# Kernel optimization log

Hardware: AMD Instinct MI355X
Metric: run time of the kernel (lower is better)

The kernel has to match this reference:

```python
import jax, jax.numpy as jnp
import numpy as np

NUM_GRAPHS = 64

def _sage(x, edge_index, Wl, bl, Wr):
    # PyG SAGEConv (mean aggr): out = lin_l(mean_{j in N(i)} x_j) + lin_r(x_i)
    src, dst = edge_index[0], edge_index[1]
    n = x.shape[0]
    summed = jax.ops.segment_sum(x[src], dst, num_segments=n)        # [N,F]
    deg = jax.ops.segment_sum(jnp.ones_like(src, dtype=x.dtype), dst, num_segments=n)
    agg = summed / jnp.maximum(deg, 1.0)[:, None]
    return agg @ Wl.T + bl + x @ Wr.T

def setup_inputs() -> dict:
    key = jax.random.key(0)
    ks = jax.random.split(key, 12)
    N, E, F, H = 50000, 600000, 128, 128
    x = jax.random.normal(ks[0], (N, F), dtype=jnp.float32)
    edge_index = jax.random.randint(ks[1], (2, E), 0, N, dtype=jnp.int64)
    batch = jnp.sort(jax.random.randint(ks[2], (N,), 0, NUM_GRAPHS, dtype=jnp.int64))
    s = lambda fan_in: 1.0 / np.sqrt(fan_in)
    return {
        "x": x, "edge_index": edge_index, "batch": batch,
        "W1l": jax.random.uniform(ks[3], (H, F), minval=-s(F), maxval=s(F)),
        "b1l": jnp.zeros((H,), jnp.float32),
        "W1r": jax.random.uniform(ks[4], (H, F), minval=-s(F), maxval=s(F)),
        "W2l": jax.random.uniform(ks[5], (H, H), minval=-s(H), maxval=s(H)),
        "b2l": jnp.zeros((H,), jnp.float32),
        "W2r": jax.random.uniform(ks[6], (H, H), minval=-s(H), maxval=s(H)),
        "Wc1": jax.random.uniform(ks[7], (H, H), minval=-s(H), maxval=s(H)),
        "bc1": jax.random.uniform(ks[8], (H,), minval=-s(H), maxval=s(H)),
        "Wc2": jax.random.uniform(ks[9], (1, H), minval=-s(H), maxval=s(H)),
        "bc2": jax.random.uniform(ks[10], (1,), minval=-s(H), maxval=s(H)),
    }

def reference(x, edge_index, batch, W1l, b1l, W1r, W2l, b2l, W2r, Wc1, bc1, Wc2, bc2):
    h = jax.nn.relu(_sage(x, edge_index, W1l, b1l, W1r))
    h = jax.nn.relu(_sage(h, edge_index, W2l, b2l, W2r))
    # global mean pool per graph
    gsum = jax.ops.segment_sum(h, batch, num_segments=NUM_GRAPHS)
    gcnt = jax.ops.segment_sum(jnp.ones((h.shape[0],), h.dtype), batch, num_segments=NUM_GRAPHS)
    gemb = gsum / jnp.maximum(gcnt, 1.0)[:, None]                    # [G,H]
    # classifier MLP (dropout = identity in eval)
    z = jax.nn.relu(gemb @ Wc1.T + bc1)
    out = (z @ Wc2.T + bc2).squeeze(-1)                              # [G]
    return out
```

## Files before the change

### kernel.cpp

```cpp
#include <hip/hip_runtime.h>


typedef __attribute__((ext_vector_type(8))) short bf16x8;
typedef __attribute__((ext_vector_type(8))) unsigned short ushort8;
typedef __attribute__((ext_vector_type(4))) float f32x4;

#define HBLK 4096

__device__ inline unsigned short f2bf(float f) {
  unsigned u = __float_as_uint(f);
  u += 0x7fff + ((u >> 16) & 1);
  return (unsigned short)(u >> 16);
}
__device__ inline float bf2f(unsigned short h) { return __uint_as_float(((unsigned)h) << 16); }


__device__ inline void wprep_body(int id, const float* __restrict__ Wl, const float* __restrict__ Wr,
                                  unsigned short* __restrict__ Bpre) {
  if (id >= 4096) return;
  int kk = id >> 9;
  int ct = (id >> 6) & 7;
  int l  = id & 63;
  int colIdx = ct * 16 + (l & 15);
  int k0 = kk * 32 + (l >> 4) * 8;
  const float* W = (k0 < 128) ? Wl : Wr;
  int kb = k0 & 127;
#pragma unroll
  for (int j = 0; j < 8; ++j) {
    float v = W[colIdx * 128 + kb + j];
    unsigned short h = f2bf(v);
    size_t bh = (size_t)kk * 8192 + ((size_t)ct * 64 + l) * 8 + j;
    Bpre[bh] = h;
    Bpre[bh + 4096] = f2bf(v - bf2f(h));
  }
}

__global__ __launch_bounds__(256) void k_prep(
    const float* __restrict__ x, unsigned short* __restrict__ xbf, int total,
    const float* __restrict__ W1l, const float* __restrict__ W1r, unsigned short* __restrict__ Bpre1,
    const float* __restrict__ W2l, const float* __restrict__ W2r, unsigned short* __restrict__ Bpre2,
    const int* __restrict__ batch, int* __restrict__ gcnt, float* __restrict__ gsum, int N,
    const int* __restrict__ ei, int* __restrict__ bhist, int E,
    int nTobf, int nEblk) {
  __shared__ int h[256];
  int b = blockIdx.x;
  int tid = threadIdx.x;
  if (b < nTobf) {
    int i = (b * 256 + tid) * 4;
    if (i + 3 < total) {
      float4 v = *(const float4*)(x + i);
      ushort4 p;
      p.x = f2bf(v.x); p.y = f2bf(v.y); p.z = f2bf(v.z); p.w = f2bf(v.w);
      *(ushort4*)(xbf + i) = p;
    } else {
      for (int k = 0; k < 4 && i + k < total; ++k) xbf[i + k] = f2bf(x[i + k]);
    }
  } else if (b < nTobf + 16) {
    wprep_body((b - nTobf) * 256 + tid, W1l, W1r, Bpre1);
  } else if (b < nTobf + 32) {
    wprep_body((b - nTobf - 16) * 256 + tid, W2l, W2r, Bpre2);
  } else if (b < nTobf + 32 + nEblk) {
    int eb = b - nTobf - 32;
    h[tid] = 0;
    __syncthreads();
    int base = eb * HBLK;
    int end = min(base + HBLK, E);
    for (int e = base + tid; e < end; e += 256) atomicAdd(&h[ei[E + e] >> 8], 1);
    __syncthreads();
    bhist[eb * 256 + tid] = h[tid];
  } else {
    for (int i = tid; i < 64 * 128; i += 256) gsum[i] = 0.f;
    if (tid < 64) {
      int g = tid;
      int lo = 0, hi = N;
      while (lo < hi) { int mid = (lo + hi) >> 1; if (batch[mid] < g) lo = mid + 1; else hi = mid; }
      int a = lo;
      lo = 0; hi = N;
      while (lo < hi) { int mid = (lo + hi) >> 1; if (batch[mid] < g + 1) lo = mid + 1; else hi = mid; }
      gcnt[g] = lo - a;
    }
  }
}


__global__ __launch_bounds__(256) void k_bscan(int* __restrict__ bhist, int* __restrict__ bukbase,
                                               int nblk) {
  __shared__ int s[256];
  int buk = blockIdx.x;
  int t = threadIdx.x;
  int sum = 0;
  for (int b = 0; b < nblk; ++b) sum += bhist[b * 256 + t];
  s[t] = sum;
  __syncthreads();
  for (int d = 1; d < 256; d <<= 1) {
    int v = (t >= d) ? s[t - d] : 0;
    __syncthreads();
    s[t] += v;
    __syncthreads();
  }
  int myBase = (buk == 0) ? 0 : s[buk - 1];
  int tot = s[255];
  __syncthreads();
  int c = (t < nblk) ? bhist[t * 256 + buk] : 0;
  s[t] = c;
  __syncthreads();
  for (int d = 1; d < 256; d <<= 1) {
    int v = (t >= d) ? s[t - d] : 0;
    __syncthreads();
    s[t] += v;
    __syncthreads();
  }
  if (t < nblk) bhist[t * 256 + buk] = myBase + s[t] - c;
  if (t == 0) bukbase[buk] = myBase;
  if (buk == 255 && t == 1) bukbase[256] = tot;
}

__global__ __launch_bounds__(256) void k_scat(const int* __restrict__ ei, const int* __restrict__ bhist,
                                              unsigned* __restrict__ ebuk, int E) {
  __shared__ int cur[256];
  int tid = threadIdx.x;
  cur[tid] = bhist[blockIdx.x * 256 + tid];
  __syncthreads();
  int base = blockIdx.x * HBLK;
  int end = min(base + HBLK, E);
  for (int e = base + tid; e < end; e += 256) {
    int d = ei[E + e];
    int srcv = ei[e];
    int p = atomicAdd(&cur[d >> 8], 1);
    ebuk[p] = ((unsigned)(d & 255) << 24) | (unsigned)srcv;
  }
}

__global__ __launch_bounds__(256) void k_bucket(const unsigned* __restrict__ ebuk,
                                                const int* __restrict__ bukbase,
                                                int* __restrict__ off, int* __restrict__ colv,
                                                int N, int E) {
  __shared__ int h[256];
  __shared__ int cur[256];
  __shared__ int sc[256];
  int tid = threadIdx.x;
  int buk = blockIdx.x;
  int b0 = bukbase[buk], b1 = bukbase[buk + 1];
  h[tid] = 0;
  __syncthreads();
  for (int i = b0 + tid; i < b1; i += 256) atomicAdd(&h[ebuk[i] >> 24], 1);
  __syncthreads();
  int my = h[tid];
  sc[tid] = my;
  __syncthreads();
  for (int d = 1; d < 256; d <<= 1) {
    int v = (tid >= d) ? sc[tid - d] : 0;
    __syncthreads();
    sc[tid] += v;
    __syncthreads();
  }
  int excl = sc[tid] - my;
  cur[tid] = excl;
  int node = buk * 256 + tid;
  if (node < N) off[node] = b0 + excl;
  if (buk == gridDim.x - 1 && tid == 0) off[N] = E;
  __syncthreads();
  for (int i = b0 + tid; i < b1; i += 256) {
    unsigned v = ebuk[i];
    int p = atomicAdd(&cur[v >> 24], 1);
    colv[b0 + p] = (int)(v & 0xFFFFFFu);
  }
}


__global__ __launch_bounds__(256) void k_agg_bf(const unsigned short* __restrict__ Xbf,
                                                const int* __restrict__ off, const int* __restrict__ col,
                                                unsigned short* __restrict__ Tbf, int N) {
  int wid = (blockIdx.x * 256 + threadIdx.x) >> 6;
  int ln = threadIdx.x & 63;
  if (wid >= N) return;
  int o0 = off[wid], o1 = off[wid + 1];
  int deg = o1 - o0;
  int rs = ln >> 4, fs = ln & 15;
  float acc[8];
#pragma unroll
  for (int j = 0; j < 8; ++j) acc[j] = 0.f;

  for (int base = 0; base < deg; base += 16) {
#pragma unroll
    for (int u = 0; u < 4; ++u) {
      int n = base + u * 4 + rs;
      if (n < deg) {
        int idx = col[o0 + n];
        ushort8 q = *(const ushort8*)(Xbf + (size_t)idx * 128 + fs * 8);
#pragma unroll
        for (int j = 0; j < 8; ++j) acc[j] += bf2f(q[j]);
      }
    }
  }
#pragma unroll
  for (int j = 0; j < 8; ++j) {
    acc[j] += __shfl_xor(acc[j], 16);
    acc[j] += __shfl_xor(acc[j], 32);
  }
  if (rs == 0) {
    float sc = 1.0f / (float)max(deg, 1);
    unsigned short w[8];
#pragma unroll
    for (int j = 0; j < 8; ++j) w[j] = f2bf(acc[j] * sc);
    uint4 uw;
    uw.x = (unsigned)w[0] | ((unsigned)w[1] << 16);
    uw.y = (unsigned)w[2] | ((unsigned)w[3] << 16);
    uw.z = (unsigned)w[4] | ((unsigned)w[5] << 16);
    uw.w = (unsigned)w[6] | ((unsigned)w[7] << 16);
    *(uint4*)(Tbf + (size_t)wid * 128 + fs * 8) = uw;
  }
}


__global__ __launch_bounds__(256) void k_lin2(
    const unsigned short* __restrict__ Agg,
    const unsigned short* __restrict__ Self,
    const unsigned short* __restrict__ Bpre,
    const float* __restrict__ bias,
    unsigned short* __restrict__ OUTbf,
    const int* __restrict__ batch, float* __restrict__ gsum,
    int N, int mode) {
  __shared__ float ps[128];
  int tid = threadIdx.x;
  int wv = tid >> 6, ln = tid & 63;
  int rowBase = blockIdx.x * 64;
  int kq = (ln >> 4) * 8;
  int rsel = ln & 15;
  int c0 = wv * 2;

  f32x4 acc[4][2];
#pragma unroll
  for (int rg = 0; rg < 4; ++rg) {
    acc[rg][0] = (f32x4){0.f, 0.f, 0.f, 0.f};
    acc[rg][1] = (f32x4){0.f, 0.f, 0.f, 0.f};
  }

#pragma unroll
  for (int kk = 0; kk < 8; ++kk) {
    const unsigned short* S = (kk < 4) ? Agg : Self;
    int kOff = (kk & 3) * 32 + kq;
    const unsigned short* Bk = Bpre + (size_t)kk * 8192;
    bf16x8 bh0 = *(const bf16x8*)(Bk + ((size_t)c0 * 64 + ln) * 8);
    bf16x8 bl0 = *(const bf16x8*)(Bk + 4096 + ((size_t)c0 * 64 + ln) * 8);
    bf16x8 bh1 = *(const bf16x8*)(Bk + ((size_t)(c0 + 1) * 64 + ln) * 8);
    bf16x8 bl1 = *(const bf16x8*)(Bk + 4096 + ((size_t)(c0 + 1) * 64 + ln) * 8);
    bf16x8 ah[4];
#pragma unroll
    for (int rg = 0; rg < 4; ++rg) {
      int row = min(rowBase + rg * 16 + rsel, N - 1);
      ah[rg] = *(const bf16x8*)(S + (size_t)row * 128 + kOff);
    }
#pragma unroll
    for (int rg = 0; rg < 4; ++rg) {
      acc[rg][0] = __builtin_amdgcn_mfma_f32_16x16x32_bf16(ah[rg], bh0, acc[rg][0], 0, 0, 0);
      acc[rg][0] = __builtin_amdgcn_mfma_f32_16x16x32_bf16(ah[rg], bl0, acc[rg][0], 0, 0, 0);
      acc[rg][1] = __builtin_amdgcn_mfma_f32_16x16x32_bf16(ah[rg], bh1, acc[rg][1], 0, 0, 0);
      acc[rg][1] = __builtin_amdgcn_mfma_f32_16x16x32_bf16(ah[rg], bl1, acc[rg][1], 0, 0, 0);
    }
  }

  int lcol = ln & 15;
  int rsub = (ln >> 4) * 4;
#pragma unroll
  for (int c = 0; c < 2; ++c) {
    float b = bias[(wv * 2 + c) * 16 + lcol];
#pragma unroll
    for (int rg = 0; rg < 4; ++rg)
#pragma unroll
      for (int r = 0; r < 4; ++r) acc[rg][c][r] = fmaxf(acc[rg][c][r] + b, 0.f);
  }

  if (mode == 0) {
#pragma unroll
    for (int rg = 0; rg < 4; ++rg)
#pragma unroll
      for (int r = 0; r < 4; ++r) {
        int row = rowBase + rg * 16 + rsub + r;
        if (row < N) {
          OUTbf[(size_t)row * 128 + (wv * 2 + 0) * 16 + lcol] = f2bf(acc[rg][0][r]);
          OUTbf[(size_t)row * 128 + (wv * 2 + 1) * 16 + lcol] = f2bf(acc[rg][1][r]);
        }
      }
  } else {
    if (tid < 128) ps[tid] = 0.f;
    __syncthreads();
    int lastRow = min(rowBase + 63, N - 1);
    int g0 = batch[rowBase], g1 = batch[lastRow];
    if (g0 == g1) {
#pragma unroll
      for (int c = 0; c < 2; ++c) {
        float s = 0.f;
#pragma unroll
        for (int rg = 0; rg < 4; ++rg)
#pragma unroll
          for (int r = 0; r < 4; ++r) {
            int row = rowBase + rg * 16 + rsub + r;
            if (row < N) s += acc[rg][c][r];
          }
        atomicAdd(&ps[(wv * 2 + c) * 16 + lcol], s);
      }
      __syncthreads();
      if (tid < 128) atomicAdd(&gsum[g0 * 128 + tid], ps[tid]);
    } else {
#pragma unroll
      for (int rg = 0; rg < 4; ++rg)
#pragma unroll
        for (int r = 0; r < 4; ++r) {
          int row = rowBase + rg * 16 + rsub + r;
          if (row < N) {
            int g = batch[row];
            atomicAdd(&gsum[g * 128 + (wv * 2 + 0) * 16 + lcol], acc[rg][0][r]);
            atomicAdd(&gsum[g * 128 + (wv * 2 + 1) * 16 + lcol], acc[rg][1][r]);
          }
        }
    }
  }
}


__global__ __launch_bounds__(128) void k_cls(const float* __restrict__ gsum, const int* __restrict__ gcnt,
                                             const float* __restrict__ Wc1, const float* __restrict__ bc1,
                                             const float* __restrict__ Wc2, const float* __restrict__ bc2,
                                             float* __restrict__ out) {
  __shared__ float red[128];
  int g = blockIdx.x;
  int h = threadIdx.x;
  float inv = 1.0f / (float)max(gcnt[g], 1);
  float s = 0.f;
  for (int f = 0; f < 128; ++f) s += gsum[g * 128 + f] * Wc1[h * 128 + f];
  red[h] = fmaxf(s * inv + bc1[h], 0.f) * Wc2[h];
  __syncthreads();
  for (int d = 64; d > 0; d >>= 1) {
    if (h < d) red[h] += red[h + d];
    __syncthreads();
  }
  if (h == 0) out[g] = red[0] + bc2[0];
}


extern "C" void kernel_launch(void* const* d_in, const int* in_sizes, int n_in,
                              void* d_out, int out_size, void* d_ws, size_t ws_size,
                              hipStream_t stream) {
  const float* x   = (const float*)d_in[0];
  const int*   ei  = (const int*)d_in[1];
  const int*   bat = (const int*)d_in[2];
  const float* W1l = (const float*)d_in[3];
  const float* b1l = (const float*)d_in[4];
  const float* W1r = (const float*)d_in[5];
  const float* W2l = (const float*)d_in[6];
  const float* b2l = (const float*)d_in[7];
  const float* W2r = (const float*)d_in[8];
  const float* Wc1 = (const float*)d_in[9];
  const float* bc1 = (const float*)d_in[10];
  const float* Wc2 = (const float*)d_in[11];
  const float* bc2 = (const float*)d_in[12];
  float* out = (float*)d_out;

  int N = in_sizes[0] / 128;
  int E = in_sizes[1] / 2;
  int nEblk = (E + HBLK - 1) / HBLK;
  int nBuk = (N + 255) >> 8;
  int total = N * 128;
  int nTobf = (total / 4 + 255) / 256;

  char* ws = (char*)d_ws;
  size_t o = 0;
  auto alloc = [&](size_t bytes) {
    char* p = ws + o;
    o += (bytes + 255) & ~(size_t)255;
    return p;
  };
  int*      off    = (int*)alloc((size_t)(N + 1) * 4);
  int*      col    = (int*)alloc((size_t)E * 4);
  unsigned* ebuk   = (unsigned*)alloc((size_t)E * 4);
  int*      bhist  = (int*)alloc((size_t)nEblk * 256 * 4);
  int*      bukbase= (int*)alloc(257 * 4);
  unsigned short* Tbf  = (unsigned short*)alloc((size_t)N * 128 * 2);
  unsigned short* xbf  = (unsigned short*)alloc((size_t)N * 128 * 2);
  unsigned short* h1bf = (unsigned short*)alloc((size_t)N * 128 * 2);
  unsigned short* Bpre1 = (unsigned short*)alloc(65536 * 2);
  unsigned short* Bpre2 = (unsigned short*)alloc(65536 * 2);
  float*    gsum   = (float*)alloc(64 * 128 * 4 + 64 * 4);
  int*      gcnt   = (int*)(gsum + 64 * 128);

  k_prep<<<nTobf + 32 + nEblk + 1, 256, 0, stream>>>(
      x, xbf, total, W1l, W1r, Bpre1, W2l, W2r, Bpre2,
      bat, gcnt, gsum, N, ei, bhist, E, nTobf, nEblk);

  k_bscan<<<256, 256, 0, stream>>>(bhist, bukbase, nEblk);
  k_scat<<<nEblk, 256, 0, stream>>>(ei, bhist, ebuk, E);
  k_bucket<<<nBuk, 256, 0, stream>>>(ebuk, bukbase, off, col, N, E);

  int nLinBlk = (N + 63) / 64;
  k_agg_bf<<<(N + 3) / 4, 256, 0, stream>>>(xbf, off, col, Tbf, N);
  k_lin2<<<nLinBlk, 256, 0, stream>>>(Tbf, xbf, Bpre1, b1l, h1bf, bat, gsum, N, 0);
  k_agg_bf<<<(N + 3) / 4, 256, 0, stream>>>(h1bf, off, col, Tbf, N);
  k_lin2<<<nLinBlk, 256, 0, stream>>>(Tbf, h1bf, Bpre2, b2l, nullptr, bat, gsum, N, 1);

  k_cls<<<64, 128, 0, stream>>>(gsum, gcnt, Wc1, bc1, Wc2, bc2, out);
}
```

Before: 181.0 us.

## Stage A and B tiles through shared memory in linear MFMA kernel

The linear-layer kernel now loads each K-slice of the activation tile and the preformatted weight tile cooperatively into LDS and reads MFMA operands from there. Before, each wave loaded its own operands straight from global memory, so every A row was fetched by all four waves. The intent is to cut redundant global loads and get coalesced 16-byte loads. In exchange it adds two barriers per K-step, a non-unrolled loop and about 20KB of LDS per block, which may lower occupancy and serialise loads with compute.

```diff
diff --git a/kernel.cpp b/kernel.cpp
--- a/kernel.cpp
+++ b/kernel.cpp
@@ -213,7 +213,7 @@
 }
 
 
-__global__ __launch_bounds__(256) void k_lin2(
+__global__ __launch_bounds__(256) void k_lin_mfma(
     const unsigned short* __restrict__ Agg,
     const unsigned short* __restrict__ Self,
     const unsigned short* __restrict__ Bpre,
@@ -221,13 +221,18 @@
     unsigned short* __restrict__ OUTbf,
     const int* __restrict__ batch, float* __restrict__ gsum,
     int N, int mode) {
+  __shared__ unsigned short As[2048];
+  __shared__ unsigned short Bs[8192];
   __shared__ float ps[128];
+
   int tid = threadIdx.x;
   int wv = tid >> 6, ln = tid & 63;
   int rowBase = blockIdx.x * 64;
-  int kq = (ln >> 4) * 8;
-  int rsel = ln & 15;
-  int c0 = wv * 2;
+
+  int sRow = tid >> 2;
+  int sKq = tid & 3;
+  int sgr = min(rowBase + sRow, N - 1);
+  int sSlot = ((sRow >> 4) * 64 + (sKq << 4) + (sRow & 15)) * 8;
 
   f32x4 acc[4][2];
 #pragma unroll
@@ -236,27 +241,38 @@
     acc[rg][1] = (f32x4){0.f, 0.f, 0.f, 0.f};
   }
 
-#pragma unroll
+  const uint4* BpreV = (const uint4*)Bpre;
+
   for (int kk = 0; kk < 8; ++kk) {
     const unsigned short* S = (kk < 4) ? Agg : Self;
-    int kOff = (kk & 3) * 32 + kq;
-    const unsigned short* Bk = Bpre + (size_t)kk * 8192;
-    bf16x8 bh0 = *(const bf16x8*)(Bk + ((size_t)c0 * 64 + ln) * 8);
-    bf16x8 bl0 = *(const bf16x8*)(Bk + 4096 + ((size_t)c0 * 64 + ln) * 8);
-    bf16x8 bh1 = *(const bf16x8*)(Bk + ((size_t)(c0 + 1) * 64 + ln) * 8);
-    bf16x8 bl1 = *(const bf16x8*)(Bk + 4096 + ((size_t)(c0 + 1) * 64 + ln) * 8);
-    bf16x8 ah[4];
+    int kOff = (kk & 3) * 32 + sKq * 8;
+    uint4 ua = *(const uint4*)(S + (size_t)sgr * 128 + kOff);
+    uint4 b0 = BpreV[kk * 1024 + tid];
+    uint4 b1 = BpreV[kk * 1024 + tid + 256];
+    uint4 b2 = BpreV[kk * 1024 + tid + 512];
+    uint4 b3 = BpreV[kk * 1024 + tid + 768];
+
+    __syncthreads();
+    *(uint4*)(As + sSlot) = ua;
+    uint4* BsV = (uint4*)Bs;
+    BsV[tid] = b0;
+    BsV[tid + 256] = b1;
+    BsV[tid + 512] = b2;
+    BsV[tid + 768] = b3;
+    __syncthreads();
+
+    int c0 = wv * 2;
+    bf16x8 bh0 = *(bf16x8*)(Bs + ((size_t)c0 * 64 + ln) * 8);
+    bf16x8 bl0 = *(bf16x8*)(Bs + 4096 + ((size_t)c0 * 64 + ln) * 8);
+    bf16x8 bh1 = *(bf16x8*)(Bs + ((size_t)(c0 + 1) * 64 + ln) * 8);
+    bf16x8 bl1 = *(bf16x8*)(Bs + 4096 + ((size_t)(c0 + 1) * 64 + ln) * 8);
 #pragma unroll
     for (int rg = 0; rg < 4; ++rg) {
-      int row = min(rowBase + rg * 16 + rsel, N - 1);
-      ah[rg] = *(const bf16x8*)(S + (size_t)row * 128 + kOff);
-    }
-#pragma unroll
-    for (int rg = 0; rg < 4; ++rg) {
-      acc[rg][0] = __builtin_amdgcn_mfma_f32_16x16x32_bf16(ah[rg], bh0, acc[rg][0], 0, 0, 0);
-      acc[rg][0] = __builtin_amdgcn_mfma_f32_16x16x32_bf16(ah[rg], bl0, acc[rg][0], 0, 0, 0);
-      acc[rg][1] = __builtin_amdgcn_mfma_f32_16x16x32_bf16(ah[rg], bh1, acc[rg][1], 0, 0, 0);
-      acc[rg][1] = __builtin_amdgcn_mfma_f32_16x16x32_bf16(ah[rg], bl1, acc[rg][1], 0, 0, 0);
+      bf16x8 ah = *(bf16x8*)(As + ((size_t)rg * 64 + ln) * 8);
+      acc[rg][0] = __builtin_amdgcn_mfma_f32_16x16x32_bf16(ah, bh0, acc[rg][0], 0, 0, 0);
+      acc[rg][0] = __builtin_amdgcn_mfma_f32_16x16x32_bf16(ah, bl0, acc[rg][0], 0, 0, 0);
+      acc[rg][1] = __builtin_amdgcn_mfma_f32_16x16x32_bf16(ah, bh1, acc[rg][1], 0, 0, 0);
+      acc[rg][1] = __builtin_amdgcn_mfma_f32_16x16x32_bf16(ah, bl1, acc[rg][1], 0, 0, 0);
     }
   }
 
@@ -394,9 +410,9 @@
 
   int nLinBlk = (N + 63) / 64;
   k_agg_bf<<<(N + 3) / 4, 256, 0, stream>>>(xbf, off, col, Tbf, N);
-  k_lin2<<<nLinBlk, 256, 0, stream>>>(Tbf, xbf, Bpre1, b1l, h1bf, bat, gsum, N, 0);
+  k_lin_mfma<<<nLinBlk, 256, 0, stream>>>(Tbf, xbf, Bpre1, b1l, h1bf, bat, gsum, N, 0);
   k_agg_bf<<<(N + 3) / 4, 256, 0, stream>>>(h1bf, off, col, Tbf, N);
-  k_lin2<<<nLinBlk, 256, 0, stream>>>(Tbf, h1bf, Bpre2, b2l, nullptr, bat, gsum, N, 1);
+  k_lin_mfma<<<nLinBlk, 256, 0, stream>>>(Tbf, h1bf, Bpre2, b2l, nullptr, bat, gsum, N, 1);
 
   k_cls<<<64, 128, 0, stream>>>(gsum, gcnt, Wc1, bc1, Wc2, bc2, out);
 }
```

Measured after the change: 163.6 us. 1.11x faster.
